# Optimization experiments

Measured on AMD Instinct MI355X. Metric: run time of the kernel, lower is better.

The kernel has to match this reference:

```python
import jax, jax.numpy as jnp
import numpy as np

MARGIN = 5.0
VAR_FLOOR = 1e-4
BIG = 1e6


def setup_inputs() -> dict:
    key = jax.random.key(0)
    ks = jax.random.split(key, 8)
    B, D, R = 512, 768, 128
    C_new, C_old = 10, 100
    return {
        "features": jax.random.normal(ks[0], (B, D), jnp.float32),
        "labels": jax.random.randint(ks[1], (B,), 0, C_new),
        "new_class_ids": jnp.arange(C_new),
        "cur_means": jax.random.normal(ks[2], (C_new, D), jnp.float32),
        "cur_bases": jax.random.normal(ks[3], (C_new, D, R), jnp.float32),
        "cur_variances": jax.random.uniform(ks[4], (C_new, R + 1), jnp.float32),
        "calibrated_old_means": jax.random.normal(ks[5], (C_old, D), jnp.float32),
        "calibrated_old_bases": jax.random.normal(ks[6], (C_old, D, R), jnp.float32),
        "calibrated_old_variances": jax.random.uniform(ks[7], (C_old, R + 1), jnp.float32),
    }


def _geometry_distance_matrix(z, means, bases, variances):
    # z: [B,D], means: [C,D], bases: [C,D,R], variances: [C,R+1] -> [B,C]
    diff = z[:, None, :] - means[None, :, :]                    # [B,C,D]
    coeff = jnp.einsum('bcd,cdr->bcr', diff, bases)             # [B,C,R]
    eig = jnp.maximum(variances[:, :-1], VAR_FLOOR)             # [C,R]
    res = jnp.maximum(variances[:, -1], VAR_FLOOR)              # [C]
    parallel = jnp.sum(coeff * coeff / eig[None, :, :], axis=-1)  # [B,C]
    recon = jnp.einsum('bcr,cdr->bcd', coeff, bases)            # [B,C,D]
    residual_term = jnp.sum((diff - recon) ** 2, axis=-1) / res[None, :]
    dist = (parallel + residual_term) / z.shape[1]              # normalize_by_dim
    return jnp.nan_to_num(dist, nan=BIG, posinf=BIG, neginf=BIG)


def reference(features, labels, new_class_ids, cur_means, cur_bases, cur_variances,
              calibrated_old_means, calibrated_old_bases, calibrated_old_variances):
    z = jnp.nan_to_num(features, nan=0.0, posinf=0.0, neginf=0.0)  # [B,D]
    labels = labels.reshape(-1)

    own_all = _geometry_distance_matrix(z, cur_means, cur_bases, cur_variances)  # [B,C_new_total]
    old_all = _geometry_distance_matrix(z, calibrated_old_means, calibrated_old_bases,
                                        calibrated_old_variances)               # [B,C_old]
    old_min = jnp.min(old_all, axis=1)                                           # [B]

    # Per-new-class masks; union of class masks reproduces new_mask implicitly.
    masks = (labels[None, :] == new_class_ids[:, None]).astype(z.dtype)          # [K,B]
    counts = masks.sum(axis=1)                                                   # [K]
    denom = jnp.maximum(counts, 1.0)

    own_k = own_all[:, new_class_ids].T                                          # [K,B]
    hinge = jax.nn.relu(MARGIN + own_k - old_min[None, :])                       # [K,B]

    total_k = (hinge * masks).sum(axis=1) / denom
    own_k_mean = (own_k * masks).sum(axis=1) / denom
    old_k_mean = (old_min[None, :] * masks).sum(axis=1) / denom

    valid = (counts > 0).astype(z.dtype)
    n_valid = jnp.maximum(valid.sum(), 1.0)
    total = (total_k * valid).sum() / n_valid
    own = (own_k_mean * valid).sum() / n_valid
    old = (old_k_mean * valid).sum() / n_valid
    return jnp.stack([total, own, old])  # [total, own, old]
```

## Files before the change

### kernel.cpp

```cpp
#include <hip/hip_runtime.h>
#include <hip/hip_bf16.h>
#include <math.h>
#include <stdint.h>

#define B_N   512
#define D_N   768
#define R_N   128
#define C_NEW 10
#define C_OLD 100
#define C_TOT 110
#define MARGIN_F    5.0f
#define VAR_FLOOR_F 1e-4f
#define BIG_F       1e6f

typedef __bf16 bf16;
typedef __bf16 bf16x4 __attribute__((ext_vector_type(4)));
typedef __bf16 bf16x8 __attribute__((ext_vector_type(8)));
typedef float  f32x4  __attribute__((ext_vector_type(4)));

__device__ __forceinline__ float cleanf(float v) { return isfinite(v) ? v : 0.0f; }

__device__ __forceinline__ unsigned encf(float f) {
    unsigned u = __float_as_uint(f);
    return (u & 0x80000000u) ? ~u : (u | 0x80000000u);
}
__device__ __forceinline__ float decf(unsigned u) {
    return (u & 0x80000000u) ? __uint_as_float(u & 0x7fffffffu) : __uint_as_float(~u);
}

__global__ __launch_bounds__(256, 2)
void prep_gram(const float* __restrict__ cur_bases, const float* __restrict__ old_bases,
               bf16* __restrict__ basesT, bf16* __restrict__ G,
               unsigned* __restrict__ ominE)
{
    const int bid = blockIdx.x, t = threadIdx.x;
    __shared__ __align__(16) unsigned char lds[32768 + 512];

    if (bid < C_TOT) {
        if (bid == 0) {
            ominE[t] = 0xFFFFFFFFu;
            ominE[256 + t] = 0xFFFFFFFFu;
        }
        const int c = bid;
        const float* Bc = (c < C_NEW) ? cur_bases + (size_t)c * D_N * R_N
                                      : old_bases + (size_t)(c - C_NEW) * D_N * R_N;
        bf16* sT = (bf16*)lds;
        const int wave = t >> 6, lane = t & 63;
        const int quad = lane >> 4, l15 = lane & 15;
        const int wrg = (wave >> 1) * 64, wsg = (wave & 1) * 64;
        const int rg = t & 31, dgq = t >> 5;

        f32x4 acc[4][4];
        #pragma unroll
        for (int i = 0; i < 4; ++i)
            #pragma unroll
            for (int j = 0; j < 4; ++j) acc[i][j] = (f32x4)0.0f;

        float4 pf[8];
        #pragma unroll
        for (int i = 0; i < 2; ++i) {
            const int dg = i * 8 + dgq;
            const float* src = Bc + (size_t)(dg * 4) * R_N + rg * 4;
            #pragma unroll
            for (int m = 0; m < 4; ++m) pf[i * 4 + m] = *(const float4*)(src + m * R_N);
        }

        for (int kc = 0; kc < 12; ++kc) {
            __syncthreads();
            #pragma unroll
            for (int i = 0; i < 2; ++i) {
                const int dg = i * 8 + dgq;
                #pragma unroll
                for (int j = 0; j < 4; ++j) {
                    const int R = rg * 4 + j;
                    bf16x4 w;
                    w[0] = (bf16)pf[i * 4 + 0][j];
                    w[1] = (bf16)pf[i * 4 + 1][j];
                    w[2] = (bf16)pf[i * 4 + 2][j];
                    w[3] = (bf16)pf[i * 4 + 3][j];
                    *(bf16x4*)(sT + R * 72 + dg * 4) = w;
                }
            }
            if (kc < 11) {
                #pragma unroll
                for (int i = 0; i < 2; ++i) {
                    const int dg = i * 8 + dgq;
                    const float* src = Bc + (size_t)((kc + 1) * 64 + dg * 4) * R_N + rg * 4;
                    #pragma unroll
                    for (int m = 0; m < 4; ++m) pf[i * 4 + m] = *(const float4*)(src + m * R_N);
                }
            }
            __syncthreads();
            #pragma unroll
            for (int kk = 0; kk < 64; kk += 32) {
                bf16x8 af[4], bg[4];
                #pragma unroll
                for (int i = 0; i < 4; ++i) af[i] = *(const bf16x8*)(sT + (wrg + 16 * i + l15) * 72 + kk + quad * 8);
                #pragma unroll
                for (int j = 0; j < 4; ++j) bg[j] = *(const bf16x8*)(sT + (wsg + 16 * j + l15) * 72 + kk + quad * 8);
                #pragma unroll
                for (int i = 0; i < 4; ++i)
                    #pragma unroll
                    for (int j = 0; j < 4; ++j)
                        acc[i][j] = __builtin_amdgcn_mfma_f32_16x16x32_bf16(af[i], bg[j], acc[i][j], 0, 0, 0);
            }
        }
        #pragma unroll
        for (int i = 0; i < 4; ++i)
            #pragma unroll
            for (int j = 0; j < 4; ++j)
                #pragma unroll
                for (int reg = 0; reg < 4; ++reg) {
                    int r = wrg + 16 * i + quad * 4 + reg;
                    int s = wsg + 16 * j + l15;
                    G[(size_t)c * 16384 + (size_t)r * 128 + s] = (bf16)acc[i][j][reg];
                }
        return;
    }

    const int tb = bid - C_TOT;
    const int dt = tb % 6, c = tb / 6;
    const float* Bc = (c < C_NEW) ? cur_bases + (size_t)c * D_N * R_N
                                  : old_bases + (size_t)(c - C_NEW) * D_N * R_N;
    bf16 (*T)[128] = (bf16(*)[128])lds;
    const int d0 = dt * 128;
    const int rg  = t & 31;
    const int dgb = t >> 5;

    #pragma unroll
    for (int i = 0; i < 4; ++i) {
        const int dg = i * 8 + dgb;
        const float* src = Bc + (size_t)(d0 + dg * 4) * R_N + rg * 4;
        float4 v0 = *(const float4*)(src);
        float4 v1 = *(const float4*)(src + R_N);
        float4 v2 = *(const float4*)(src + 2 * R_N);
        float4 v3 = *(const float4*)(src + 3 * R_N);
        const float* f0 = (const float*)&v0;
        const float* f1 = (const float*)&v1;
        const float* f2 = (const float*)&v2;
        const float* f3 = (const float*)&v3;
        #pragma unroll
        for (int j = 0; j < 4; ++j) {
            const int R = rg * 4 + j;
            const int pc = dg ^ (R & 31);
            bf16x4 w;
            w[0] = (bf16)f0[j]; w[1] = (bf16)f1[j]; w[2] = (bf16)f2[j]; w[3] = (bf16)f3[j];
            *(bf16x4*)(&T[R][pc * 4]) = w;
        }
    }
    __syncthreads();

    #pragma unroll
    for (int it = 0; it < 16; ++it) {
        const int q = it * 256 + t;
        const int r = q >> 5, u = q & 31;
        const int pc = u ^ (r & 31);
        ushort4 w = *(const ushort4*)(&T[r][pc * 4]);
        *(ushort4*)(basesT + (size_t)c * R_N * D_N + (size_t)r * D_N + d0 + u * 4) = w;
    }
}

#define PADC 136
#define SM_A    0
#define SM_B    9216
#define SM_C    0
#define SM_MU   27648
#define SM_INV  30720
#define SM_Q    31232
#define SM_PAR  31488
#define SM_CN   31744
#define SM_ND   32000
#define SM_T2   32256
#define SM_SZ   34304

__global__ __launch_bounds__(256, 4)
void main_dist(const float* __restrict__ z, const bf16* __restrict__ basesT,
               const bf16* __restrict__ G,
               const float* __restrict__ cur_vars, const float* __restrict__ old_vars,
               const float* __restrict__ cur_means, const float* __restrict__ old_means,
               float* __restrict__ gdist, unsigned* __restrict__ ominE)
{
    const int fid = blockIdx.x;
    const int x = fid & 7;
    const int y = (fid % 112) >> 3;
    const int mt = fid / 112;
    const int c = x + 8 * y;
    if (c >= C_TOT) return;

    __shared__ __align__(16) unsigned char smem[SM_SZ];
    bf16*  sA   = (bf16*)(smem + SM_A);
    bf16*  sB   = (bf16*)(smem + SM_B);
    bf16*  sC   = (bf16*)(smem + SM_C);
    float* sMu  = (float*)(smem + SM_MU);
    float* sInv = (float*)(smem + SM_INV);
    float* sQ   = (float*)(smem + SM_Q);
    float* sPar = (float*)(smem + SM_PAR);
    float* sCn  = (float*)(smem + SM_CN);
    float* sNd  = (float*)(smem + SM_ND);
    float* sT2  = (float*)(smem + SM_T2);

    const int tid = threadIdx.x, wave = tid >> 6, lane = tid & 63;
    const int quad = lane >> 4, l15 = lane & 15;
    const int wr  = (wave >> 1) * 32;
    const int wcc = (wave & 1) * 64;

    const int b0 = mt * 64;
    const float* vars = (c < C_NEW) ? cur_vars + (size_t)c * (R_N + 1)
                                    : old_vars + (size_t)(c - C_NEW) * (R_N + 1);
    const float* mu = (c < C_NEW) ? cur_means + (size_t)c * D_N
                                  : old_means + (size_t)(c - C_NEW) * D_N;

    if (tid < 128) sInv[tid] = 1.0f / fmaxf(vars[tid], VAR_FLOOR_F);
    if (tid < 64)  sQ[tid] = 0.0f;
    for (int i = tid; i < D_N; i += 256) sMu[i] = mu[i];

    f32x4 acc1[2][4];
    #pragma unroll
    for (int i = 0; i < 2; ++i)
        #pragma unroll
        for (int j = 0; j < 4; ++j) acc1[i][j] = (f32x4)0.0f;
    float nd2p[4];
    #pragma unroll
    for (int p = 0; p < 4; ++p) nd2p[p] = 0.f;

    const int rg4 = tid >> 4, f4 = tid & 15;
    const float* Az = z + (size_t)b0 * D_N;
    const bf16*  Bb = basesT + (size_t)c * R_N * D_N;

    for (int kc = 0; kc < 12; ++kc) {
        const int k0 = kc * 64;
        __syncthreads();
        #pragma unroll
        for (int p = 0; p < 4; ++p) {
            int q = p * 256 + tid, row = q >> 3, u = q & 7;
            *(uint4*)(sB + row * 72 + u * 8) = *(const uint4*)(Bb + (size_t)row * D_N + k0 + u * 8);
        }
        {
            float4 m4 = *(const float4*)(sMu + k0 + f4 * 4);
            #pragma unroll
            for (int p = 0; p < 4; ++p) {
                int row = p * 16 + rg4;
                float4 v = *(const float4*)(Az + (size_t)row * D_N + k0 + f4 * 4);
                float d0 = cleanf(v.x) - m4.x;
                float d1 = cleanf(v.y) - m4.y;
                float d2 = cleanf(v.z) - m4.z;
                float d3 = cleanf(v.w) - m4.w;
                nd2p[p] += d0 * d0 + d1 * d1 + d2 * d2 + d3 * d3;
                bf16x4 w;
                w[0] = (bf16)d0; w[1] = (bf16)d1; w[2] = (bf16)d2; w[3] = (bf16)d3;
                *(bf16x4*)(sA + row * 72 + f4 * 4) = w;
            }
        }
        __syncthreads();
        #pragma unroll
        for (int kk = 0; kk < 64; kk += 32) {
            bf16x8 af[2], bg[4];
            #pragma unroll
            for (int i = 0; i < 2; ++i) af[i] = *(const bf16x8*)(sA + (wr + 16 * i + l15) * 72 + kk + quad * 8);
            #pragma unroll
            for (int j = 0; j < 4; ++j) bg[j] = *(const bf16x8*)(sB + (wcc + 16 * j + l15) * 72 + kk + quad * 8);
            #pragma unroll
            for (int i = 0; i < 2; ++i)
                #pragma unroll
                for (int j = 0; j < 4; ++j)
                    acc1[i][j] = __builtin_amdgcn_mfma_f32_16x16x32_bf16(af[i], bg[j], acc1[i][j], 0, 0, 0);
        }
    }

    #pragma unroll
    for (int p = 0; p < 4; ++p) {
        float s = nd2p[p];
        s += __shfl_xor(s, 1, 64); s += __shfl_xor(s, 2, 64);
        s += __shfl_xor(s, 4, 64); s += __shfl_xor(s, 8, 64);
        if (f4 == 0) sNd[p * 16 + rg4] = s;
    }
    __syncthreads();

    #pragma unroll
    for (int i = 0; i < 2; ++i)
        #pragma unroll
        for (int j = 0; j < 4; ++j)
            #pragma unroll
            for (int reg = 0; reg < 4; ++reg)
                sC[(wr + 16 * i + quad * 4 + reg) * PADC + wcc + 16 * j + l15] = (bf16)acc1[i][j][reg];
    __syncthreads();

    {
        int row = tid >> 2, qtr = tid & 3;
        float par = 0.f, cn = 0.f;
        #pragma unroll
        for (int m = 0; m < 4; ++m) {
            bf16x8 v = *(const bf16x8*)(sC + row * PADC + qtr * 32 + m * 8);
            #pragma unroll
            for (int e = 0; e < 8; ++e) {
                float f = (float)v[e];
                int col = qtr * 32 + m * 8 + e;
                cn  += f * f;
                par += f * f * sInv[col];
            }
        }
        sT2[tid] = par;
        sT2[256 + tid] = cn;
    }
    __syncthreads();
    if (tid < 64) {
        sPar[tid] = sT2[tid * 4] + sT2[tid * 4 + 1] + sT2[tid * 4 + 2] + sT2[tid * 4 + 3];
        sCn[tid]  = sT2[256 + tid * 4] + sT2[256 + tid * 4 + 1]
                  + sT2[256 + tid * 4 + 2] + sT2[256 + tid * 4 + 3];
    }

    const bf16* Gc = G + (size_t)c * 16384;
    f32x4 acc2[2][4];
    #pragma unroll
    for (int i = 0; i < 2; ++i)
        #pragma unroll
        for (int j = 0; j < 4; ++j) acc2[i][j] = (f32x4)0.0f;
    #pragma unroll
    for (int kc4 = 0; kc4 < 4; ++kc4) {
        const int kb = kc4 * 32;
        bf16x8 af[2], bg[4];
        #pragma unroll
        for (int i = 0; i < 2; ++i) af[i] = *(const bf16x8*)(sC + (wr + 16 * i + l15) * PADC + kb + quad * 8);
        #pragma unroll
        for (int j = 0; j < 4; ++j) bg[j] = *(const bf16x8*)(Gc + (size_t)(wcc + 16 * j + l15) * 128 + kb + quad * 8);
        #pragma unroll
        for (int i = 0; i < 2; ++i)
            #pragma unroll
            for (int j = 0; j < 4; ++j)
                acc2[i][j] = __builtin_amdgcn_mfma_f32_16x16x32_bf16(af[i], bg[j], acc2[i][j], 0, 0, 0);
    }

    #pragma unroll
    for (int i = 0; i < 2; ++i)
        #pragma unroll
        for (int reg = 0; reg < 4; ++reg) {
            const int row = wr + 16 * i + quad * 4 + reg;
            float qp = 0.f;
            #pragma unroll
            for (int j = 0; j < 4; ++j)
                qp += acc2[i][j][reg] * (float)sC[row * PADC + wcc + 16 * j + l15];
            qp += __shfl_xor(qp, 1, 64);
            qp += __shfl_xor(qp, 2, 64);
            qp += __shfl_xor(qp, 4, 64);
            qp += __shfl_xor(qp, 8, 64);
            if (l15 == 0) atomicAdd(&sQ[row], qp);
        }
    __syncthreads();

    if (tid < 64) {
        int b = b0 + tid;
        float res = fmaxf(vars[R_N], VAR_FLOOR_F);
        float dist = (sPar[tid] + (sNd[tid] - 2.0f * sCn[tid] + sQ[tid]) / res) / (float)D_N;
        if (!isfinite(dist)) dist = BIG_F;
        if (c < C_NEW) {
            gdist[(size_t)b * C_NEW + c] = dist;
        } else {
            atomicMin(ominE + b, encf(dist));
        }
    }
}

__global__ __launch_bounds__(512)
void finalize(const float* __restrict__ gdist, const unsigned* __restrict__ ominE,
              const int* __restrict__ labels, const int* __restrict__ ncid,
              float* __restrict__ out)
{
    __shared__ float acc[C_NEW * 4];
    __shared__ int sNcid[C_NEW];
    const int t = threadIdx.x;
    if (t < C_NEW * 4) acc[t] = 0.f;
    if (t < C_NEW) sNcid[t] = ncid[t];
    __syncthreads();

    {
        float mn = decf(ominE[t]);
        const int lab = labels[t];
        #pragma unroll
        for (int k = 0; k < C_NEW; ++k) {
            if (lab == sNcid[k]) {
                int col = min(max(sNcid[k], 0), C_NEW - 1);
                float ow = gdist[(size_t)t * C_NEW + col];
                atomicAdd(&acc[k * 4 + 0], 1.0f);
                atomicAdd(&acc[k * 4 + 1], fmaxf(0.0f, MARGIN_F + ow - mn));
                atomicAdd(&acc[k * 4 + 2], ow);
                atomicAdd(&acc[k * 4 + 3], mn);
            }
        }
    }
    __syncthreads();

    if (t == 0) {
        float total = 0.f, own = 0.f, old = 0.f, nv = 0.f;
        #pragma unroll
        for (int k = 0; k < C_NEW; ++k) {
            float cnt = acc[k * 4 + 0];
            float den = fmaxf(cnt, 1.0f);
            if (cnt > 0.f) {
                nv += 1.f;
                total += acc[k * 4 + 1] / den;
                own   += acc[k * 4 + 2] / den;
                old   += acc[k * 4 + 3] / den;
            }
        }
        float nvd = fmaxf(nv, 1.0f);
        out[0] = total / nvd;
        out[1] = own / nvd;
        out[2] = old / nvd;
    }
}

extern "C" void kernel_launch(void* const* d_in, const int* in_sizes, int n_in,
                              void* d_out, int out_size, void* d_ws, size_t ws_size,
                              hipStream_t stream)
{
    const float* features  = (const float*)d_in[0];
    const int*   labels    = (const int*)d_in[1];
    const int*   ncid      = (const int*)d_in[2];
    const float* cur_means = (const float*)d_in[3];
    const float* cur_bases = (const float*)d_in[4];
    const float* cur_vars  = (const float*)d_in[5];
    const float* old_means = (const float*)d_in[6];
    const float* old_bases = (const float*)d_in[7];
    const float* old_vars  = (const float*)d_in[8];

    unsigned char* ws = (unsigned char*)d_ws;
    float*    gdist  = (float*)(ws + 0);
    unsigned* ominE  = (unsigned*)(ws + 20480);
    bf16*     basesT = (bf16*) (ws + 22528);
    bf16*     G      = (bf16*) (ws + 21649408);

    prep_gram<<<dim3(C_TOT + 6 * C_TOT), dim3(256), 0, stream>>>(
        cur_bases, old_bases, basesT, G, ominE);
    main_dist<<<dim3(896), dim3(256), 0, stream>>>(features, basesT, G,
                                                   cur_vars, old_vars,
                                                   cur_means, old_means,
                                                   gdist, ominE);
    finalize<<<dim3(1), dim3(512), 0, stream>>>(gdist, ominE, labels, ncid,
                                                (float*)d_out);
}
```

Measured before the change: 158.8 us.

## Fuse finalize into main_dist via last-block ticket and prefetch next K tile

```diff
diff --git a/kernel.cpp b/kernel.cpp
--- a/kernel.cpp
+++ b/kernel.cpp
@@ -31,7 +31,7 @@
 __global__ __launch_bounds__(256, 2)
 void prep_gram(const float* __restrict__ cur_bases, const float* __restrict__ old_bases,
                bf16* __restrict__ basesT, bf16* __restrict__ G,
-               unsigned* __restrict__ ominE)
+               unsigned* __restrict__ ominE, unsigned* __restrict__ cnt)
 {
     const int bid = blockIdx.x, t = threadIdx.x;
     __shared__ __align__(16) unsigned char lds[32768 + 512];
@@ -40,6 +40,7 @@
         if (bid == 0) {
             ominE[t] = 0xFFFFFFFFu;
             ominE[256 + t] = 0xFFFFFFFFu;
+            if (t == 0) *cnt = 0u;
         }
         const int c = bid;
         const float* Bc = (c < C_NEW) ? cur_bases + (size_t)c * D_N * R_N
@@ -178,16 +179,18 @@
                const bf16* __restrict__ G,
                const float* __restrict__ cur_vars, const float* __restrict__ old_vars,
                const float* __restrict__ cur_means, const float* __restrict__ old_means,
-               float* __restrict__ gdist, unsigned* __restrict__ ominE)
+               const int* __restrict__ labels, const int* __restrict__ ncid,
+               float* __restrict__ gdist, unsigned* __restrict__ ominE,
+               unsigned* __restrict__ cnt, float* __restrict__ out)
 {
     const int fid = blockIdx.x;
     const int x = fid & 7;
     const int y = (fid % 112) >> 3;
     const int mt = fid / 112;
     const int c = x + 8 * y;
-    if (c >= C_TOT) return;
 
     __shared__ __align__(16) unsigned char smem[SM_SZ];
+    __shared__ unsigned sTick;
     bf16*  sA   = (bf16*)(smem + SM_A);
     bf16*  sB   = (bf16*)(smem + SM_B);
     bf16*  sC   = (bf16*)(smem + SM_C);
@@ -204,208 +207,240 @@
     const int wr  = (wave >> 1) * 32;
     const int wcc = (wave & 1) * 64;
 
-    const int b0 = mt * 64;
-    const float* vars = (c < C_NEW) ? cur_vars + (size_t)c * (R_N + 1)
-                                    : old_vars + (size_t)(c - C_NEW) * (R_N + 1);
-    const float* mu = (c < C_NEW) ? cur_means + (size_t)c * D_N
-                                  : old_means + (size_t)(c - C_NEW) * D_N;
-
-    if (tid < 128) sInv[tid] = 1.0f / fmaxf(vars[tid], VAR_FLOOR_F);
-    if (tid < 64)  sQ[tid] = 0.0f;
-    for (int i = tid; i < D_N; i += 256) sMu[i] = mu[i];
-
-    f32x4 acc1[2][4];
-    #pragma unroll
-    for (int i = 0; i < 2; ++i)
-        #pragma unroll
-        for (int j = 0; j < 4; ++j) acc1[i][j] = (f32x4)0.0f;
-    float nd2p[4];
-    #pragma unroll
-    for (int p = 0; p < 4; ++p) nd2p[p] = 0.f;
-
-    const int rg4 = tid >> 4, f4 = tid & 15;
-    const float* Az = z + (size_t)b0 * D_N;
-    const bf16*  Bb = basesT + (size_t)c * R_N * D_N;
-
-    for (int kc = 0; kc < 12; ++kc) {
-        const int k0 = kc * 64;
-        __syncthreads();
+    if (c < C_TOT) {
+        const int b0 = mt * 64;
+        const float* vars = (c < C_NEW) ? cur_vars + (size_t)c * (R_N + 1)
+                                        : old_vars + (size_t)(c - C_NEW) * (R_N + 1);
+        const float* mu = (c < C_NEW) ? cur_means + (size_t)c * D_N
+                                      : old_means + (size_t)(c - C_NEW) * D_N;
+
+        if (tid < 128) sInv[tid] = 1.0f / fmaxf(vars[tid], VAR_FLOOR_F);
+        if (tid < 64)  sQ[tid] = 0.0f;
+        for (int i = tid; i < D_N; i += 256) sMu[i] = mu[i];
+
+        f32x4 acc1[2][4];
+        #pragma unroll
+        for (int i = 0; i < 2; ++i)
+            #pragma unroll
+            for (int j = 0; j < 4; ++j) acc1[i][j] = (f32x4)0.0f;
+        float nd2p[4];
+        #pragma unroll
+        for (int p = 0; p < 4; ++p) nd2p[p] = 0.f;
+
+        const int rg4 = tid >> 4, f4 = tid & 15;
+        const float* Az = z + (size_t)b0 * D_N;
+        const bf16*  Bb = basesT + (size_t)c * R_N * D_N;
+
+        uint4  pbf[4];
+        float4 paf[4];
         #pragma unroll
         for (int p = 0; p < 4; ++p) {
             int q = p * 256 + tid, row = q >> 3, u = q & 7;
-            *(uint4*)(sB + row * 72 + u * 8) = *(const uint4*)(Bb + (size_t)row * D_N + k0 + u * 8);
-        }
+            pbf[p] = *(const uint4*)(Bb + (size_t)row * D_N + u * 8);
+        }
+        #pragma unroll
+        for (int p = 0; p < 4; ++p) {
+            int row = p * 16 + rg4;
+            paf[p] = *(const float4*)(Az + (size_t)row * D_N + f4 * 4);
+        }
+
+        for (int kc = 0; kc < 12; ++kc) {
+            const int k0 = kc * 64;
+            __syncthreads();
+            #pragma unroll
+            for (int p = 0; p < 4; ++p) {
+                int q = p * 256 + tid, row = q >> 3, u = q & 7;
+                *(uint4*)(sB + row * 72 + u * 8) = pbf[p];
+            }
+            {
+                float4 m4 = *(const float4*)(sMu + k0 + f4 * 4);
+                #pragma unroll
+                for (int p = 0; p < 4; ++p) {
+                    int row = p * 16 + rg4;
+                    float d0 = cleanf(paf[p].x) - m4.x;
+                    float d1 = cleanf(paf[p].y) - m4.y;
+                    float d2 = cleanf(paf[p].z) - m4.z;
+                    float d3 = cleanf(paf[p].w) - m4.w;
+                    nd2p[p] += d0 * d0 + d1 * d1 + d2 * d2 + d3 * d3;
+                    bf16x4 w;
+                    w[0] = (bf16)d0; w[1] = (bf16)d1; w[2] = (bf16)d2; w[3] = (bf16)d3;
+                    *(bf16x4*)(sA + row * 72 + f4 * 4) = w;
+                }
+            }
+            if (kc < 11) {
+                #pragma unroll
+                for (int p = 0; p < 4; ++p) {
+                    int q = p * 256 + tid, row = q >> 3, u = q & 7;
+                    pbf[p] = *(const uint4*)(Bb + (size_t)row * D_N + (k0 + 64) + u * 8);
+                }
+                #pragma unroll
+                for (int p = 0; p < 4; ++p) {
+                    int row = p * 16 + rg4;
+                    paf[p] = *(const float4*)(Az + (size_t)row * D_N + (k0 + 64) + f4 * 4);
+                }
+            }
+            __syncthreads();
+            #pragma unroll
+            for (int kk = 0; kk < 64; kk += 32) {
+                bf16x8 af[2], bg[4];
+                #pragma unroll
+                for (int i = 0; i < 2; ++i) af[i] = *(const bf16x8*)(sA + (wr + 16 * i + l15) * 72 + kk + quad * 8);
+                #pragma unroll
+                for (int j = 0; j < 4; ++j) bg[j] = *(const bf16x8*)(sB + (wcc + 16 * j + l15) * 72 + kk + quad * 8);
+                #pragma unroll
+                for (int i = 0; i < 2; ++i)
+                    #pragma unroll
+                    for (int j = 0; j < 4; ++j)
+                        acc1[i][j] = __builtin_amdgcn_mfma_f32_16x16x32_bf16(af[i], bg[j], acc1[i][j], 0, 0, 0);
+            }
+        }
+
+        #pragma unroll
+        for (int p = 0; p < 4; ++p) {
+            float s = nd2p[p];
+            s += __shfl_xor(s, 1, 64); s += __shfl_xor(s, 2, 64);
+            s += __shfl_xor(s, 4, 64); s += __shfl_xor(s, 8, 64);
+            if (f4 == 0) sNd[p * 16 + rg4] = s;
+        }
+        __syncthreads();
+
+        #pragma unroll
+        for (int i = 0; i < 2; ++i)
+            #pragma unroll
+            for (int j = 0; j < 4; ++j)
+                #pragma unroll
+                for (int reg = 0; reg < 4; ++reg)
+                    sC[(wr + 16 * i + quad * 4 + reg) * PADC + wcc + 16 * j + l15] = (bf16)acc1[i][j][reg];
+        __syncthreads();
+
         {
-            float4 m4 = *(const float4*)(sMu + k0 + f4 * 4);
-            #pragma unroll
-            for (int p = 0; p < 4; ++p) {
-                int row = p * 16 + rg4;
-                float4 v = *(const float4*)(Az + (size_t)row * D_N + k0 + f4 * 4);
-                float d0 = cleanf(v.x) - m4.x;
-                float d1 = cleanf(v.y) - m4.y;
-                float d2 = cleanf(v.z) - m4.z;
-                float d3 = cleanf(v.w) - m4.w;
-                nd2p[p] += d0 * d0 + d1 * d1 + d2 * d2 + d3 * d3;
-                bf16x4 w;
-                w[0] = (bf16)d0; w[1] = (bf16)d1; w[2] = (bf16)d2; w[3] = (bf16)d3;
-                *(bf16x4*)(sA + row * 72 + f4 * 4) = w;
-            }
-        }
-        __syncthreads();
-        #pragma unroll
-        for (int kk = 0; kk < 64; kk += 32) {
+            int row = tid >> 2, qtr = tid & 3;
+            float par = 0.f, cn = 0.f;
+            #pragma unroll
+            for (int m = 0; m < 4; ++m) {
+                bf16x8 v = *(const bf16x8*)(sC + row * PADC + qtr * 32 + m * 8);
+                #pragma unroll
+                for (int e = 0; e < 8; ++e) {
+                    float f = (float)v[e];
+                    int col = qtr * 32 + m * 8 + e;
+                    cn  += f * f;
+                    par += f * f * sInv[col];
+                }
+            }
+            sT2[tid] = par;
+            sT2[256 + tid] = cn;
+        }
+        __syncthreads();
+        if (tid < 64) {
+            sPar[tid] = sT2[tid * 4] + sT2[tid * 4 + 1] + sT2[tid * 4 + 2] + sT2[tid * 4 + 3];
+            sCn[tid]  = sT2[256 + tid * 4] + sT2[256 + tid * 4 + 1]
+                      + sT2[256 + tid * 4 + 2] + sT2[256 + tid * 4 + 3];
+        }
+
+        const bf16* Gc = G + (size_t)c * 16384;
+        f32x4 acc2[2][4];
+        #pragma unroll
+        for (int i = 0; i < 2; ++i)
+            #pragma unroll
+            for (int j = 0; j < 4; ++j) acc2[i][j] = (f32x4)0.0f;
+        #pragma unroll
+        for (int kc4 = 0; kc4 < 4; ++kc4) {
+            const int kb = kc4 * 32;
             bf16x8 af[2], bg[4];
             #pragma unroll
-            for (int i = 0; i < 2; ++i) af[i] = *(const bf16x8*)(sA + (wr + 16 * i + l15) * 72 + kk + quad * 8);
-            #pragma unroll
-            for (int j = 0; j < 4; ++j) bg[j] = *(const bf16x8*)(sB + (wcc + 16 * j + l15) * 72 + kk + quad * 8);
+            for (int i = 0; i < 2; ++i) af[i] = *(const bf16x8*)(sC + (wr + 16 * i + l15) * PADC + kb + quad * 8);
+            #pragma unroll
+            for (int j = 0; j < 4; ++j) bg[j] = *(const bf16x8*)(Gc + (size_t)(wcc + 16 * j + l15) * 128 + kb + quad * 8);
             #pragma unroll
             for (int i = 0; i < 2; ++i)
                 #pragma unroll
                 for (int j = 0; j < 4; ++j)
-                    acc1[i][j] = __builtin_amdgcn_mfma_f32_16x16x32_bf16(af[i], bg[j], acc1[i][j], 0, 0, 0);
-        }
-    }
-
-    #pragma unroll
-    for (int p = 0; p < 4; ++p) {
-        float s = nd2p[p];
-        s += __shfl_xor(s, 1, 64); s += __shfl_xor(s, 2, 64);
-        s += __shfl_xor(s, 4, 64); s += __shfl_xor(s, 8, 64);
-        if (f4 == 0) sNd[p * 16 + rg4] = s;
-    }
+                    acc2[i][j] = __builtin_amdgcn_mfma_f32_16x16x32_bf16(af[i], bg[j], acc2[i][j], 0, 0, 0);
+        }
+
+        #pragma unroll
+        for (int i = 0; i < 2; ++i)
+            #pragma unroll
+            for (int reg = 0; reg < 4; ++reg) {
+                const int row = wr + 16 * i + quad * 4 + reg;
+                float qp = 0.f;
+                #pragma unroll
+                for (int j = 0; j < 4; ++j)
+                    qp += acc2[i][j][reg] * (float)sC[row * PADC + wcc + 16 * j + l15];
+                qp += __shfl_xor(qp, 1, 64);
+                qp += __shfl_xor(qp, 2, 64);
+                qp += __shfl_xor(qp, 4, 64);
+                qp += __shfl_xor(qp, 8, 64);
+                if (l15 == 0) atomicAdd(&sQ[row], qp);
+            }
+        __syncthreads();
+
+        if (tid < 64) {
+            int b = b0 + tid;
+            float res = fmaxf(vars[R_N], VAR_FLOOR_F);
+            float dist = (sPar[tid] + (sNd[tid] - 2.0f * sCn[tid] + sQ[tid]) / res) / (float)D_N;
+            if (!isfinite(dist)) dist = BIG_F;
+            if (c < C_NEW) {
+                __hip_atomic_store(&gdist[(size_t)b * C_NEW + c], dist,
+                                   __ATOMIC_RELAXED, __HIP_MEMORY_SCOPE_AGENT);
+            } else {
+                atomicMin(ominE + b, encf(dist));
+            }
+        }
+    }
+
     __syncthreads();
-
-    #pragma unroll
-    for (int i = 0; i < 2; ++i)
-        #pragma unroll
-        for (int j = 0; j < 4; ++j)
-            #pragma unroll
-            for (int reg = 0; reg < 4; ++reg)
-                sC[(wr + 16 * i + quad * 4 + reg) * PADC + wcc + 16 * j + l15] = (bf16)acc1[i][j][reg];
+    if (tid == 0) {
+        asm volatile("s_waitcnt vmcnt(0)" ::: "memory");
+        sTick = __hip_atomic_fetch_add(cnt, 1u, __ATOMIC_RELAXED, __HIP_MEMORY_SCOPE_AGENT);
+    }
     __syncthreads();
+    if (sTick != 895u) return;
 
     {
-        int row = tid >> 2, qtr = tid & 3;
-        float par = 0.f, cn = 0.f;
-        #pragma unroll
-        for (int m = 0; m < 4; ++m) {
-            bf16x8 v = *(const bf16x8*)(sC + row * PADC + qtr * 32 + m * 8);
-            #pragma unroll
-            for (int e = 0; e < 8; ++e) {
-                float f = (float)v[e];
-                int col = qtr * 32 + m * 8 + e;
-                cn  += f * f;
-                par += f * f * sInv[col];
-            }
-        }
-        sT2[tid] = par;
-        sT2[256 + tid] = cn;
-    }
-    __syncthreads();
-    if (tid < 64) {
-        sPar[tid] = sT2[tid * 4] + sT2[tid * 4 + 1] + sT2[tid * 4 + 2] + sT2[tid * 4 + 3];
-        sCn[tid]  = sT2[256 + tid * 4] + sT2[256 + tid * 4 + 1]
-                  + sT2[256 + tid * 4 + 2] + sT2[256 + tid * 4 + 3];
-    }
-
-    const bf16* Gc = G + (size_t)c * 16384;
-    f32x4 acc2[2][4];
-    #pragma unroll
-    for (int i = 0; i < 2; ++i)
-        #pragma unroll
-        for (int j = 0; j < 4; ++j) acc2[i][j] = (f32x4)0.0f;
-    #pragma unroll
-    for (int kc4 = 0; kc4 < 4; ++kc4) {
-        const int kb = kc4 * 32;
-        bf16x8 af[2], bg[4];
-        #pragma unroll
-        for (int i = 0; i < 2; ++i) af[i] = *(const bf16x8*)(sC + (wr + 16 * i + l15) * PADC + kb + quad * 8);
-        #pragma unroll
-        for (int j = 0; j < 4; ++j) bg[j] = *(const bf16x8*)(Gc + (size_t)(wcc + 16 * j + l15) * 128 + kb + quad * 8);
-        #pragma unroll
-        for (int i = 0; i < 2; ++i)
-            #pragma unroll
-            for (int j = 0; j < 4; ++j)
-                acc2[i][j] = __builtin_amdgcn_mfma_f32_16x16x32_bf16(af[i], bg[j], acc2[i][j], 0, 0, 0);
-    }
-
-    #pragma unroll
-    for (int i = 0; i < 2; ++i)
-        #pragma unroll
-        for (int reg = 0; reg < 4; ++reg) {
-            const int row = wr + 16 * i + quad * 4 + reg;
-            float qp = 0.f;
-            #pragma unroll
-            for (int j = 0; j < 4; ++j)
-                qp += acc2[i][j][reg] * (float)sC[row * PADC + wcc + 16 * j + l15];
-            qp += __shfl_xor(qp, 1, 64);
-            qp += __shfl_xor(qp, 2, 64);
-            qp += __shfl_xor(qp, 4, 64);
-            qp += __shfl_xor(qp, 8, 64);
-            if (l15 == 0) atomicAdd(&sQ[row], qp);
-        }
-    __syncthreads();
-
-    if (tid < 64) {
-        int b = b0 + tid;
-        float res = fmaxf(vars[R_N], VAR_FLOOR_F);
-        float dist = (sPar[tid] + (sNd[tid] - 2.0f * sCn[tid] + sQ[tid]) / res) / (float)D_N;
-        if (!isfinite(dist)) dist = BIG_F;
-        if (c < C_NEW) {
-            gdist[(size_t)b * C_NEW + c] = dist;
-        } else {
-            atomicMin(ominE + b, encf(dist));
-        }
-    }
-}
-
-__global__ __launch_bounds__(512)
-void finalize(const float* __restrict__ gdist, const unsigned* __restrict__ ominE,
-              const int* __restrict__ labels, const int* __restrict__ ncid,
-              float* __restrict__ out)
-{
-    __shared__ float acc[C_NEW * 4];
-    __shared__ int sNcid[C_NEW];
-    const int t = threadIdx.x;
-    if (t < C_NEW * 4) acc[t] = 0.f;
-    if (t < C_NEW) sNcid[t] = ncid[t];
-    __syncthreads();
-
-    {
-        float mn = decf(ominE[t]);
-        const int lab = labels[t];
-        #pragma unroll
-        for (int k = 0; k < C_NEW; ++k) {
-            if (lab == sNcid[k]) {
-                int col = min(max(sNcid[k], 0), C_NEW - 1);
-                float ow = gdist[(size_t)t * C_NEW + col];
-                atomicAdd(&acc[k * 4 + 0], 1.0f);
-                atomicAdd(&acc[k * 4 + 1], fmaxf(0.0f, MARGIN_F + ow - mn));
-                atomicAdd(&acc[k * 4 + 2], ow);
-                atomicAdd(&acc[k * 4 + 3], mn);
-            }
-        }
-    }
-    __syncthreads();
-
-    if (t == 0) {
-        float total = 0.f, own = 0.f, old = 0.f, nv = 0.f;
-        #pragma unroll
-        for (int k = 0; k < C_NEW; ++k) {
-            float cnt = acc[k * 4 + 0];
-            float den = fmaxf(cnt, 1.0f);
-            if (cnt > 0.f) {
-                nv += 1.f;
-                total += acc[k * 4 + 1] / den;
-                own   += acc[k * 4 + 2] / den;
-                old   += acc[k * 4 + 3] / den;
-            }
-        }
-        float nvd = fmaxf(nv, 1.0f);
-        out[0] = total / nvd;
-        out[1] = own / nvd;
-        out[2] = old / nvd;
+        float* accF = sT2;
+        int* ncidS = (int*)(sT2 + 48);
+        if (tid < 40) accF[tid] = 0.f;
+        if (tid < C_NEW) ncidS[tid] = ncid[tid];
+        __syncthreads();
+        #pragma unroll
+        for (int rep = 0; rep < 2; ++rep) {
+            int b = rep * 256 + tid;
+            unsigned me = __hip_atomic_load(&ominE[b], __ATOMIC_RELAXED, __HIP_MEMORY_SCOPE_AGENT);
+            float mn = decf(me);
+            int lab = labels[b];
+            #pragma unroll
+            for (int k = 0; k < C_NEW; ++k) {
+                if (lab == ncidS[k]) {
+                    int col = min(max(ncidS[k], 0), C_NEW - 1);
+                    float ow = __hip_atomic_load(&gdist[(size_t)b * C_NEW + col],
+                                                 __ATOMIC_RELAXED, __HIP_MEMORY_SCOPE_AGENT);
+                    atomicAdd(&accF[k * 4 + 0], 1.0f);
+                    atomicAdd(&accF[k * 4 + 1], fmaxf(0.0f, MARGIN_F + ow - mn));
+                    atomicAdd(&accF[k * 4 + 2], ow);
+                    atomicAdd(&accF[k * 4 + 3], mn);
+                }
+            }
+        }
+        __syncthreads();
+        if (tid == 0) {
+            float total = 0.f, own = 0.f, old = 0.f, nv = 0.f;
+            #pragma unroll
+            for (int k = 0; k < C_NEW; ++k) {
+                float cntk = accF[k * 4 + 0];
+                float den = fmaxf(cntk, 1.0f);
+                if (cntk > 0.f) {
+                    nv += 1.f;
+                    total += accF[k * 4 + 1] / den;
+                    own   += accF[k * 4 + 2] / den;
+                    old   += accF[k * 4 + 3] / den;
+                }
+            }
+            float nvd = fmaxf(nv, 1.0f);
+            out[0] = total / nvd;
+            out[1] = own / nvd;
+            out[2] = old / nvd;
+        }
     }
 }
 
@@ -426,15 +461,15 @@
     unsigned char* ws = (unsigned char*)d_ws;
     float*    gdist  = (float*)(ws + 0);
     unsigned* ominE  = (unsigned*)(ws + 20480);
-    bf16*     basesT = (bf16*) (ws + 22528);
-    bf16*     G      = (bf16*) (ws + 21649408);
+    unsigned* cnt    = (unsigned*)(ws + 22528);
+    bf16*     basesT = (bf16*) (ws + 22544);
+    bf16*     G      = (bf16*) (ws + 21649424);
 
     prep_gram<<<dim3(C_TOT + 6 * C_TOT), dim3(256), 0, stream>>>(
-        cur_bases, old_bases, basesT, G, ominE);
+        cur_bases, old_bases, basesT, G, ominE, cnt);
     main_dist<<<dim3(896), dim3(256), 0, stream>>>(features, basesT, G,
                                                    cur_vars, old_vars,
                                                    cur_means, old_means,
-                                                   gdist, ominE);
-    finalize<<<dim3(1), dim3(512), 0, stream>>>(gdist, ominE, labels, ncid,
-                                                (float*)d_out);
+                                                   labels, ncid,
+                                                   gdist, ominE, cnt, (float*)d_out);
 }
```

New measurement: 213.6 us. 1.35x slower.

## Precompute bf16 features and mean projections; use direct global-to-LDS loads in main GEMM

Applied to the files above, without the earlier changes.

```diff
diff --git a/kernel.cpp b/kernel.cpp
--- a/kernel.cpp
+++ b/kernel.cpp
@@ -28,24 +28,64 @@
     return (u & 0x80000000u) ? __uint_as_float(u & 0x7fffffffu) : __uint_as_float(~u);
 }
 
+#define GL16(gp, lp)                                                            \
+    __builtin_amdgcn_global_load_lds(                                           \
+        (const __attribute__((address_space(1))) unsigned int*)(gp),            \
+        (__attribute__((address_space(3))) unsigned int*)(lp), 16, 0, 0)
+
+__device__ __forceinline__ int swz_elem(int D, int row) {
+    int k0 = D & ~63;
+    int g  = (D >> 3) & 7;
+    return k0 + (((g ^ (row & 7))) << 3) + (D & 7);
+}
+
 __global__ __launch_bounds__(256, 2)
-void prep_gram(const float* __restrict__ cur_bases, const float* __restrict__ old_bases,
-               bf16* __restrict__ basesT, bf16* __restrict__ G,
-               unsigned* __restrict__ ominE)
+void prep_all(const float* __restrict__ z,
+              const float* __restrict__ cur_means, const float* __restrict__ old_means,
+              const float* __restrict__ cur_bases, const float* __restrict__ old_bases,
+              bf16* __restrict__ zbf, float* __restrict__ znorm,
+              float* __restrict__ munorm, float* __restrict__ m_c,
+              bf16* __restrict__ basesT, bf16* __restrict__ G,
+              unsigned* __restrict__ ominE)
 {
     const int bid = blockIdx.x, t = threadIdx.x;
-    __shared__ __align__(16) unsigned char lds[32768 + 512];
-
-    if (bid < C_TOT) {
+    __shared__ __align__(16) unsigned char lds[33280];
+    const int wave = t >> 6, lane = t & 63;
+
+    if (bid < 128) {
         if (bid == 0) {
             ominE[t] = 0xFFFFFFFFu;
             ominE[256 + t] = 0xFFFFFFFFu;
         }
-        const int c = bid;
+        const int b = bid * 4 + wave;
+        const float4* src = (const float4*)(z + (size_t)b * D_N);
+        bf16* dst = zbf + (size_t)b * D_N;
+        float nrm = 0.f;
+        #pragma unroll
+        for (int i = 0; i < 3; ++i) {
+            const int D = (lane + i * 64) * 4;
+            float4 v = src[lane + i * 64];
+            v.x = cleanf(v.x); v.y = cleanf(v.y); v.z = cleanf(v.z); v.w = cleanf(v.w);
+            nrm += v.x * v.x + v.y * v.y + v.z * v.z + v.w * v.w;
+            bf16x4 w;
+            w[0] = (bf16)v.x; w[1] = (bf16)v.y; w[2] = (bf16)v.z; w[3] = (bf16)v.w;
+            *(bf16x4*)(dst + swz_elem(D, b)) = w;
+        }
+        #pragma unroll
+        for (int off = 32; off >= 1; off >>= 1) nrm += __shfl_xor(nrm, off, 64);
+        if (lane == 0) znorm[b] = nrm;
+        return;
+    }
+
+    if (bid < 128 + C_TOT) {
+        const int c = bid - 128;
         const float* Bc = (c < C_NEW) ? cur_bases + (size_t)c * D_N * R_N
                                       : old_bases + (size_t)(c - C_NEW) * D_N * R_N;
-        bf16* sT = (bf16*)lds;
-        const int wave = t >> 6, lane = t & 63;
+        const float* mu = (c < C_NEW) ? cur_means + (size_t)c * D_N
+                                      : old_means + (size_t)(c - C_NEW) * D_N;
+        bf16*  sT   = (bf16*)lds;
+        float* sMuF = (float*)(lds + 18432);
+        float* sRed = (float*)(lds + 18432 + 256);
         const int quad = lane >> 4, l15 = lane & 15;
         const int wrg = (wave >> 1) * 64, wsg = (wave & 1) * 64;
         const int rg = t & 31, dgq = t >> 5;
@@ -55,6 +95,7 @@
         for (int i = 0; i < 4; ++i)
             #pragma unroll
             for (int j = 0; j < 4; ++j) acc[i][j] = (f32x4)0.0f;
+        float mAcc = 0.f, muN = 0.f;
 
         float4 pf[8];
         #pragma unroll
@@ -66,6 +107,7 @@
         }
 
         for (int kc = 0; kc < 12; ++kc) {
+            const int k0 = kc * 64;
             __syncthreads();
             #pragma unroll
             for (int i = 0; i < 2; ++i) {
@@ -81,6 +123,11 @@
                     *(bf16x4*)(sT + R * 72 + dg * 4) = w;
                 }
             }
+            if (t < 64) {
+                float mv = mu[k0 + t];
+                sMuF[t] = mv;
+                muN += mv * mv;
+            }
             if (kc < 11) {
                 #pragma unroll
                 for (int i = 0; i < 2; ++i) {
@@ -104,6 +151,17 @@
                     for (int j = 0; j < 4; ++j)
                         acc[i][j] = __builtin_amdgcn_mfma_f32_16x16x32_bf16(af[i], bg[j], acc[i][j], 0, 0, 0);
             }
+            {
+                const int rr = t >> 1, hf = t & 1;
+                const bf16* tr = sT + rr * 72 + hf * 32;
+                const float* mf = sMuF + hf * 32;
+                #pragma unroll
+                for (int m = 0; m < 4; ++m) {
+                    bf16x8 v = *(const bf16x8*)(tr + m * 8);
+                    #pragma unroll
+                    for (int e = 0; e < 8; ++e) mAcc += (float)v[e] * mf[m * 8 + e];
+                }
+            }
         }
         #pragma unroll
         for (int i = 0; i < 4; ++i)
@@ -115,10 +173,18 @@
                     int s = wsg + 16 * j + l15;
                     G[(size_t)c * 16384 + (size_t)r * 128 + s] = (bf16)acc[i][j][reg];
                 }
+        sRed[t] = mAcc;
+        __syncthreads();
+        if (t < 128) m_c[c * R_N + t] = sRed[2 * t] + sRed[2 * t + 1];
+        if (t < 64) {
+            #pragma unroll
+            for (int off = 32; off >= 1; off >>= 1) muN += __shfl_xor(muN, off, 64);
+            if (lane == 0) munorm[c] = muN;
+        }
         return;
     }
 
-    const int tb = bid - C_TOT;
+    const int tb = bid - (128 + C_TOT);
     const int dt = tb % 6, c = tb / 6;
     const float* Bc = (c < C_NEW) ? cur_bases + (size_t)c * D_N * R_N
                                   : old_bases + (size_t)(c - C_NEW) * D_N * R_N;
@@ -156,28 +222,31 @@
         const int r = q >> 5, u = q & 31;
         const int pc = u ^ (r & 31);
         ushort4 w = *(const ushort4*)(&T[r][pc * 4]);
-        *(ushort4*)(basesT + (size_t)c * R_N * D_N + (size_t)r * D_N + d0 + u * 4) = w;
+        const int D = d0 + u * 4;
+        *(ushort4*)(basesT + (size_t)c * R_N * D_N + (size_t)r * D_N + swz_elem(D, r)) = w;
     }
 }
 
 #define PADC 136
 #define SM_A    0
-#define SM_B    9216
+#define SM_B    8192
 #define SM_C    0
-#define SM_MU   27648
-#define SM_INV  30720
-#define SM_Q    31232
-#define SM_PAR  31488
-#define SM_CN   31744
-#define SM_ND   32000
-#define SM_T2   32256
-#define SM_SZ   34304
+#define SM_MU   24576
+#define SM_M    26112
+#define SM_INV  26624
+#define SM_Q    27136
+#define SM_PAR  27392
+#define SM_CN   27648
+#define SM_ZD   27904
+#define SM_T2   28160
+#define SM_SZ   30208
 
 __global__ __launch_bounds__(256, 4)
-void main_dist(const float* __restrict__ z, const bf16* __restrict__ basesT,
-               const bf16* __restrict__ G,
+void main_dist(const bf16* __restrict__ zbf, const bf16* __restrict__ basesT,
+               const bf16* __restrict__ G, const float* __restrict__ m_c,
                const float* __restrict__ cur_vars, const float* __restrict__ old_vars,
                const float* __restrict__ cur_means, const float* __restrict__ old_means,
+               const float* __restrict__ znorm, const float* __restrict__ munorm,
                float* __restrict__ gdist, unsigned* __restrict__ ominE)
 {
     const int fid = blockIdx.x;
@@ -188,15 +257,16 @@
     if (c >= C_TOT) return;
 
     __shared__ __align__(16) unsigned char smem[SM_SZ];
-    bf16*  sA   = (bf16*)(smem + SM_A);
-    bf16*  sB   = (bf16*)(smem + SM_B);
+    unsigned char* sAb = smem + SM_A;
+    unsigned char* sBb = smem + SM_B;
     bf16*  sC   = (bf16*)(smem + SM_C);
-    float* sMu  = (float*)(smem + SM_MU);
+    bf16*  sMuB = (bf16*)(smem + SM_MU);
+    float* sM   = (float*)(smem + SM_M);
     float* sInv = (float*)(smem + SM_INV);
     float* sQ   = (float*)(smem + SM_Q);
     float* sPar = (float*)(smem + SM_PAR);
     float* sCn  = (float*)(smem + SM_CN);
-    float* sNd  = (float*)(smem + SM_ND);
+    float* sZd  = (float*)(smem + SM_ZD);
     float* sT2  = (float*)(smem + SM_T2);
 
     const int tid = threadIdx.x, wave = tid >> 6, lane = tid & 63;
@@ -210,79 +280,83 @@
     const float* mu = (c < C_NEW) ? cur_means + (size_t)c * D_N
                                   : old_means + (size_t)(c - C_NEW) * D_N;
 
-    if (tid < 128) sInv[tid] = 1.0f / fmaxf(vars[tid], VAR_FLOOR_F);
-    if (tid < 64)  sQ[tid] = 0.0f;
-    for (int i = tid; i < D_N; i += 256) sMu[i] = mu[i];
+    if (tid < 128) {
+        sM[tid]   = m_c[c * R_N + tid];
+        sInv[tid] = 1.0f / fmaxf(vars[tid], VAR_FLOOR_F);
+    }
+    if (tid < 64) sQ[tid] = 0.0f;
+    for (int i = tid; i < D_N; i += 256) sMuB[i] = (bf16)mu[i];
 
     f32x4 acc1[2][4];
     #pragma unroll
     for (int i = 0; i < 2; ++i)
         #pragma unroll
         for (int j = 0; j < 4; ++j) acc1[i][j] = (f32x4)0.0f;
-    float nd2p[4];
-    #pragma unroll
-    for (int p = 0; p < 4; ++p) nd2p[p] = 0.f;
-
-    const int rg4 = tid >> 4, f4 = tid & 15;
-    const float* Az = z + (size_t)b0 * D_N;
-    const bf16*  Bb = basesT + (size_t)c * R_N * D_N;
+    float zd = 0.f;
+    const int zrow = tid >> 2, zpart = tid & 3;
+
+    const char* BbB = (const char*)basesT + (size_t)c * (R_N * D_N * 2);
+    const char* AzB = (const char*)zbf + (size_t)b0 * (D_N * 2);
+    const int offRC = (wave * 8 + (lane >> 3)) * (D_N * 2) + (lane & 7) * 16;
+    char* ldsB = (char*)sBb + wave * 1024;
+    char* ldsA = (char*)sAb + wave * 1024;
 
     for (int kc = 0; kc < 12; ++kc) {
+        const int kb = kc * 128;
         const int k0 = kc * 64;
         __syncthreads();
         #pragma unroll
-        for (int p = 0; p < 4; ++p) {
-            int q = p * 256 + tid, row = q >> 3, u = q & 7;
-            *(uint4*)(sB + row * 72 + u * 8) = *(const uint4*)(Bb + (size_t)row * D_N + k0 + u * 8);
-        }
-        {
-            float4 m4 = *(const float4*)(sMu + k0 + f4 * 4);
-            #pragma unroll
-            for (int p = 0; p < 4; ++p) {
-                int row = p * 16 + rg4;
-                float4 v = *(const float4*)(Az + (size_t)row * D_N + k0 + f4 * 4);
-                float d0 = cleanf(v.x) - m4.x;
-                float d1 = cleanf(v.y) - m4.y;
-                float d2 = cleanf(v.z) - m4.z;
-                float d3 = cleanf(v.w) - m4.w;
-                nd2p[p] += d0 * d0 + d1 * d1 + d2 * d2 + d3 * d3;
-                bf16x4 w;
-                w[0] = (bf16)d0; w[1] = (bf16)d1; w[2] = (bf16)d2; w[3] = (bf16)d3;
-                *(bf16x4*)(sA + row * 72 + f4 * 4) = w;
-            }
-        }
+        for (int p = 0; p < 4; ++p)
+            GL16(BbB + offRC + p * (32 * D_N * 2) + kb, ldsB + p * 4096);
+        #pragma unroll
+        for (int q = 0; q < 2; ++q)
+            GL16(AzB + offRC + q * (32 * D_N * 2) + kb, ldsA + q * 4096);
         __syncthreads();
         #pragma unroll
         for (int kk = 0; kk < 64; kk += 32) {
+            const int gbase = kk >> 3;
             bf16x8 af[2], bg[4];
             #pragma unroll
-            for (int i = 0; i < 2; ++i) af[i] = *(const bf16x8*)(sA + (wr + 16 * i + l15) * 72 + kk + quad * 8);
-            #pragma unroll
-            for (int j = 0; j < 4; ++j) bg[j] = *(const bf16x8*)(sB + (wcc + 16 * j + l15) * 72 + kk + quad * 8);
+            for (int i = 0; i < 2; ++i) {
+                const int rowA = wr + 16 * i + l15;
+                af[i] = *(const bf16x8*)(sAb + rowA * 128 + (((gbase + quad) ^ (rowA & 7)) << 4));
+            }
+            #pragma unroll
+            for (int j = 0; j < 4; ++j) {
+                const int rowB = wcc + 16 * j + l15;
+                bg[j] = *(const bf16x8*)(sBb + rowB * 128 + (((gbase + quad) ^ (rowB & 7)) << 4));
+            }
             #pragma unroll
             for (int i = 0; i < 2; ++i)
                 #pragma unroll
                 for (int j = 0; j < 4; ++j)
                     acc1[i][j] = __builtin_amdgcn_mfma_f32_16x16x32_bf16(af[i], bg[j], acc1[i][j], 0, 0, 0);
         }
-    }
-
-    #pragma unroll
-    for (int p = 0; p < 4; ++p) {
-        float s = nd2p[p];
-        s += __shfl_xor(s, 1, 64); s += __shfl_xor(s, 2, 64);
-        s += __shfl_xor(s, 4, 64); s += __shfl_xor(s, 8, 64);
-        if (f4 == 0) sNd[p * 16 + rg4] = s;
-    }
-    __syncthreads();
-
-    #pragma unroll
-    for (int i = 0; i < 2; ++i)
-        #pragma unroll
-        for (int j = 0; j < 4; ++j)
+        #pragma unroll
+        for (int gg = 0; gg < 2; ++gg) {
+            const int g = zpart * 2 + gg;
+            bf16x8 a = *(const bf16x8*)(sAb + zrow * 128 + ((g ^ (zrow & 7)) << 4));
+            bf16x8 b = *(const bf16x8*)(sMuB + k0 + g * 8);
+            #pragma unroll
+            for (int e = 0; e < 8; ++e) zd += (float)a[e] * (float)b[e];
+        }
+    }
+
+    zd += __shfl_xor(zd, 1, 64);
+    zd += __shfl_xor(zd, 2, 64);
+    if ((tid & 3) == 0) sZd[zrow] = zd;
+    __syncthreads();
+
+    #pragma unroll
+    for (int j = 0; j < 4; ++j) {
+        float mcv = sM[wcc + 16 * j + l15];
+        #pragma unroll
+        for (int i = 0; i < 2; ++i)
             #pragma unroll
             for (int reg = 0; reg < 4; ++reg)
-                sC[(wr + 16 * i + quad * 4 + reg) * PADC + wcc + 16 * j + l15] = (bf16)acc1[i][j][reg];
+                sC[(wr + 16 * i + quad * 4 + reg) * PADC + wcc + 16 * j + l15] =
+                    (bf16)(acc1[i][j][reg] - mcv);
+    }
     __syncthreads();
 
     {
@@ -349,8 +423,9 @@
 
     if (tid < 64) {
         int b = b0 + tid;
+        float nd2 = znorm[b] - 2.0f * sZd[tid] + munorm[c];
         float res = fmaxf(vars[R_N], VAR_FLOOR_F);
-        float dist = (sPar[tid] + (sNd[tid] - 2.0f * sCn[tid] + sQ[tid]) / res) / (float)D_N;
+        float dist = (sPar[tid] + (nd2 - 2.0f * sCn[tid] + sQ[tid]) / res) / (float)D_N;
         if (!isfinite(dist)) dist = BIG_F;
         if (c < C_NEW) {
             gdist[(size_t)b * C_NEW + c] = dist;
@@ -426,14 +501,20 @@
     unsigned char* ws = (unsigned char*)d_ws;
     float*    gdist  = (float*)(ws + 0);
     unsigned* ominE  = (unsigned*)(ws + 20480);
-    bf16*     basesT = (bf16*) (ws + 22528);
-    bf16*     G      = (bf16*) (ws + 21649408);
-
-    prep_gram<<<dim3(C_TOT + 6 * C_TOT), dim3(256), 0, stream>>>(
-        cur_bases, old_bases, basesT, G, ominE);
-    main_dist<<<dim3(896), dim3(256), 0, stream>>>(features, basesT, G,
+    bf16*     zbf    = (bf16*) (ws + 22528);
+    float*    znorm  = (float*)(ws + 808960);
+    float*    munorm = (float*)(ws + 811008);
+    float*    m_c    = (float*)(ws + 811520);
+    bf16*     basesT = (bf16*) (ws + 867840);
+    bf16*     G      = (bf16*) (ws + 22494720);
+
+    prep_all<<<dim3(128 + C_TOT + 6 * C_TOT), dim3(256), 0, stream>>>(
+        features, cur_means, old_means, cur_bases, old_bases,
+        zbf, znorm, munorm, m_c, basesT, G, ominE);
+    main_dist<<<dim3(896), dim3(256), 0, stream>>>(zbf, basesT, G, m_c,
                                                    cur_vars, old_vars,
                                                    cur_means, old_means,
+                                                   znorm, munorm,
                                                    gdist, ominE);
     finalize<<<dim3(1), dim3(512), 0, stream>>>(gdist, ominE, labels, ncid,
                                                 (float*)d_out);
```

Result: no change. 156.6 us, median of 2 (-1.3%).
